# Kernel optimization log

Measured on AMD Instinct MI355X. Metric: run time of the kernel, lower is better.

The kernel has to match this reference:

```python
import jax, jax.numpy as jnp
from jax import lax
import numpy as np

# ---- static APPM geometry (MMAL-Net config: input 448, stride 32 -> 14x14 fm) ----
STRIDE = 32
FM = 14
RATIOS = [[4, 4], [3, 5], [5, 3],
          [6, 6], [5, 7], [7, 5],
          [8, 8], [6, 10], [10, 6], [7, 9], [9, 7], [7, 10], [10, 7]]
N_LIST = [3, 2, 1]          # proposals per ratio-group -> proposalN = 6
IOU_THRESHS = [0.25, 0.25, 0.25]
GROUP_RATIO_SPLITS = [3, 6, 13]  # ratios 0:3, 3:6, 6:13


def _window_num(r):
    return (FM - r[0] + 1) * (FM - r[1] + 1)


def _build_coords():
    # indices2coordinates: window (i,j) of ratio (rh,rw) -> pixel box, inclusive ends
    coords = []
    for rh, rw in RATIOS:
        rows, cols = FM - rh + 1, FM - rw + 1
        ii, jj = np.meshgrid(np.arange(rows), np.arange(cols), indexing='ij')
        x0 = ii.reshape(-1) * STRIDE
        y0 = jj.reshape(-1) * STRIDE
        x1 = x0 + rh * STRIDE - 1
        y1 = y0 + rw * STRIDE - 1
        coords.append(np.stack([x0, y0, x1, y1], 1))
    return np.concatenate(coords, 0).astype(np.float32)

COORDS = jnp.asarray(_build_coords())  # [917, 4]
WINDOW_NUMS = [_window_num(r) for r in RATIOS]
_g1 = sum(WINDOW_NUMS[:3]); _g2 = sum(WINDOW_NUMS[3:6]); _g3 = sum(WINDOW_NUMS[6:])
GROUPS = [(0, _g1), (_g1, _g1 + _g2), (_g1 + _g2, _g1 + _g2 + _g3)]  # (0,361),(361,602),(602,917)


def _argmax_mask(logits):
    # mask = 0.7 everywhere, 1.0 at per-row argmax
    B, C = logits.shape
    one_hot = jax.nn.one_hot(jnp.argmax(logits, axis=1), C, dtype=logits.dtype)
    return 0.7 + 0.3 * one_hot


def _nms_group(scores, coords, n_pick, thresh):
    # greedy descending-score NMS; scores [W], coords [W,4]
    x0, y0, x1, y1 = coords[:, 0], coords[:, 1], coords[:, 2], coords[:, 3]
    areas = (x1 - x0 + 1.0) * (y1 - y0 + 1.0)

    def step(carry, _):
        valid, last = carry
        masked = jnp.where(valid, scores, -jnp.inf)
        idx = jnp.argmax(masked).astype(jnp.int32)
        idx = jnp.where(valid.any(), idx, last)  # pad by repeating last pick
        ix0, iy0, ix1, iy1 = coords[idx]
        lx = jnp.minimum(x1, ix1) - jnp.maximum(x0, ix0) + 1.0
        ly = jnp.minimum(y1, iy1) - jnp.maximum(y0, iy0) + 1.0
        inter = jnp.where((lx < 0) | (ly < 0), 0.0, lx * ly)
        iou = inter / (areas + areas[idx] - inter)
        valid = valid & (iou <= thresh)  # also suppresses idx itself (iou == 1)
        return (valid, idx), idx

    init = (jnp.ones(scores.shape[0], dtype=bool), jnp.int32(0))
    (_, _), picks = lax.scan(step, init, None, length=n_pick)
    return picks  # [n_pick] int32


def _appm(local_fm):
    # avgpool over each ratio then sum over channels == channel-sum then 2D mean pool
    B = local_fm.shape[0]
    fm_sum = jnp.sum(local_fm, axis=1)  # [B,14,14]
    per_ratio = []
    for rh, rw in RATIOS:
        pooled = lax.reduce_window(fm_sum, jnp.float32(0.0), lax.add,
                                   (1, rh, rw), (1, 1, 1), 'VALID') / (rh * rw)
        per_ratio.append(pooled.reshape(B, -1))
    all_scores = jnp.concatenate(per_ratio, axis=1)  # [B, 917]

    picks = []
    for (s, e), n_pick, thr in zip(GROUPS, N_LIST, IOU_THRESHS):
        g = jax.vmap(lambda sc: _nms_group(sc, COORDS[s:e], n_pick, thr))(all_scores[:, s:e])
        picks.append(g + s)
    proposalN_indices = jnp.concatenate(picks, axis=1)  # [B, 6]
    proposalN_windows_scores = jnp.take_along_axis(all_scores, proposalN_indices, axis=1)
    return proposalN_indices, proposalN_windows_scores, all_scores


def setup_inputs() -> dict:
    key = jax.random.key(0)
    ks = jax.random.split(key, 6)
    B, C, NC, BIT = 256, 512, 200, 48
    return {
        'local_fm': jax.random.normal(ks[0], (B, C, 14, 14), jnp.float32),
        'local_embeddings': jax.random.normal(ks[1], (B, C), jnp.float32),
        'W_cls': jax.random.normal(ks[2], (NC, C), jnp.float32) * 0.02,
        'b_cls': jax.random.normal(ks[3], (NC,), jnp.float32) * 0.02,
        'W_hash': jax.random.normal(ks[4], (BIT, NC), jnp.float32) * 0.02,
        'b_hash': jax.random.normal(ks[5], (BIT,), jnp.float32) * 0.02,
    }


def reference(local_fm, local_embeddings, W_cls, b_cls, W_hash, b_hash):
    # classification head + per-row argmax masking + hash head (Tanh)
    local_logits = local_embeddings @ W_cls.T + b_cls          # [B, num_classes]
    masked = local_logits * _argmax_mask(local_logits)
    local_hash_code = jnp.tanh(masked @ W_hash.T + b_hash)     # [B, bit]
    # APPM region proposal on detached feature map
    proposalN_indices, proposalN_windows_scores, window_scores = _appm(
        lax.stop_gradient(local_fm))
    return (local_hash_code, local_logits, proposalN_indices,
            proposalN_windows_scores, window_scores)
```

## Files before the change

### kernel.cpp

```cpp
#include <hip/hip_runtime.h>
#include <math.h>

#define NW 917

__constant__ int c_off[13]  = {0,121,241,361,442,522,602,651,696,741,789,837,877};
__constant__ int c_rh[13]   = {4,3,5,6,5,7,8,6,10,7,9,7,10};
__constant__ int c_rw[13]   = {4,5,3,6,7,5,8,10,6,9,7,10,7};
__constant__ int c_cols[13] = {11,10,12,9,8,10,7,5,9,6,8,5,8};

__device__ inline void decode_w(int w, int& r, int& i, int& j){
    int rr = 0;
    #pragma unroll
    for (int k = 1; k < 13; ++k) if (w >= c_off[k]) rr = k;
    int loc = w - c_off[rr];
    int cols = c_cols[rr];
    r = rr; i = loc / cols; j = loc - i * cols;
}

__global__ __launch_bounds__(512) void chansum_kernel(const float* __restrict__ fm,
                                                      float* __restrict__ fmsum){
    int b = blockIdx.x;
    int t = threadIdx.x;
    int sub = t >> 6, lane = t & 63;
    __shared__ float4 red[8][49];
    const float4* base = (const float4*)(fm + (size_t)b * 512 * 196);
    if (lane < 49){
        float4 acc = {0.f,0.f,0.f,0.f};
        int c0 = sub * 64;
        #pragma unroll 8
        for (int c = 0; c < 64; ++c){
            float4 v = base[(size_t)(c0 + c) * 49 + lane];
            acc.x += v.x; acc.y += v.y; acc.z += v.z; acc.w += v.w;
        }
        red[sub][lane] = acc;
    }
    __syncthreads();
    if (t < 49){
        float4 s = red[0][t];
        #pragma unroll
        for (int k = 1; k < 8; ++k){
            float4 v = red[k][t];
            s.x += v.x; s.y += v.y; s.z += v.z; s.w += v.w;
        }
        ((float4*)fmsum)[b * 49 + t] = s;
    }
}

__global__ __launch_bounds__(256) void appm_kernel(const float* __restrict__ fmsum,
                                                   float* __restrict__ out_scores,
                                                   float* __restrict__ out_idx,
                                                   float* __restrict__ out_psc){
    int b = blockIdx.x, t = threadIdx.x;
    __shared__ float fm[196];
    __shared__ float R[14][15];
    __shared__ float I[15][15];
    __shared__ float s[NW];
    __shared__ float rv[256];
    __shared__ int   ri[256];

    if (t < 196) fm[t] = fmsum[b * 196 + t];
    __syncthreads();
    if (t < 14){
        float run = 0.f;
        R[t][0] = 0.f;
        for (int j = 0; j < 14; ++j){ run += fm[t * 14 + j]; R[t][j + 1] = run; }
    }
    __syncthreads();
    if (t < 15){
        float run = 0.f;
        I[0][t] = 0.f;
        for (int i = 0; i < 14; ++i){ run += R[i][t]; I[i + 1][t] = run; }
    }
    __syncthreads();
    for (int w = t; w < NW; w += 256){
        int r, i, j; decode_w(w, r, i, j);
        int rh = c_rh[r], rw = c_rw[r];
        float sum = I[i + rh][j + rw] - I[i][j + rw] - I[i + rh][j] + I[i][j];
        float sc = sum / (float)(rh * rw);
        s[w] = sc;
        out_scores[(size_t)b * NW + w] = sc;
    }
    __syncthreads();

    const int gs_[3] = {0, 361, 602};
    const int ge_[3] = {361, 602, NW};
    const int np_[3] = {3, 2, 1};
    int slot = 0;
    for (int g = 0; g < 3; ++g){
        int gs = gs_[g], ge = ge_[g];
        int w0 = gs + t, w1 = gs + t + 256;
        bool has0 = w0 < ge, has1 = w1 < ge;
        float x00=0,y00=0,x10=0,y10=0,a0=1.f;
        float x01=0,y01=0,x11=0,y11=0,a1=1.f;
        if (has0){
            int r,i,j; decode_w(w0,r,i,j);
            x00 = i*32.f; y00 = j*32.f;
            x10 = x00 + c_rh[r]*32.f - 1.f; y10 = y00 + c_rw[r]*32.f - 1.f;
            a0  = (float)(c_rh[r]*32 * c_rw[r]*32);
        }
        if (has1){
            int r,i,j; decode_w(w1,r,i,j);
            x01 = i*32.f; y01 = j*32.f;
            x11 = x01 + c_rh[r]*32.f - 1.f; y11 = y01 + c_rw[r]*32.f - 1.f;
            a1  = (float)(c_rh[r]*32 * c_rw[r]*32);
        }
        bool v0 = true, v1 = true;
        int last = 0;
        for (int p = 0; p < np_[g]; ++p){
            float bv = -INFINITY; int bi = 0x7fffffff;
            if (has0 && v0){ bv = s[w0]; bi = w0; }
            if (has1 && v1){ float sv = s[w1]; if (sv > bv){ bv = sv; bi = w1; } }
            rv[t] = bv; ri[t] = bi;
            __syncthreads();
            for (int st = 128; st > 0; st >>= 1){
                if (t < st){
                    float ov = rv[t + st]; int oi = ri[t + st];
                    if (ov > rv[t] || (ov == rv[t] && oi < ri[t])){ rv[t] = ov; ri[t] = oi; }
                }
                __syncthreads();
            }
            float mv = rv[0];
            int pick = (mv == -INFINITY) ? last : ri[0];
            __syncthreads();
            last = pick;
            int pr, pi, pj; decode_w(pick, pr, pi, pj);
            float px0 = pi*32.f, py0 = pj*32.f;
            float px1 = px0 + c_rh[pr]*32.f - 1.f, py1 = py0 + c_rw[pr]*32.f - 1.f;
            float pa  = (float)(c_rh[pr]*32 * c_rw[pr]*32);
            if (has0 && v0){
                float lx = fminf(x10,px1) - fmaxf(x00,px0) + 1.f;
                float ly = fminf(y10,py1) - fmaxf(y00,py0) + 1.f;
                float inter = (lx < 0.f || ly < 0.f) ? 0.f : lx * ly;
                float iou = inter / (a0 + pa - inter);
                v0 = (iou <= 0.25f);
            }
            if (has1 && v1){
                float lx = fminf(x11,px1) - fmaxf(x01,px0) + 1.f;
                float ly = fminf(y11,py1) - fmaxf(y01,py0) + 1.f;
                float inter = (lx < 0.f || ly < 0.f) ? 0.f : lx * ly;
                float iou = inter / (a1 + pa - inter);
                v1 = (iou <= 0.25f);
            }
            if (t == 0){
                out_idx[b * 6 + slot] = (float)pick;
                out_psc[b * 6 + slot] = s[pick];
            }
            slot++;
        }
    }
}

__global__ __launch_bounds__(256) void cls_kernel(const float* __restrict__ E,
                                                  const float* __restrict__ Wc,
                                                  const float* __restrict__ bc,
                                                  const float* __restrict__ Wh,
                                                  const float* __restrict__ bh,
                                                  float* __restrict__ out_hash,
                                                  float* __restrict__ out_logits){
    int b = blockIdx.x, t = threadIdx.x;
    __shared__ float emb[512];
    __shared__ float lg[200];
    __shared__ float mk[200];
    __shared__ float rv[256];
    __shared__ int   ri[256];
    emb[t]       = E[b * 512 + t];
    emb[t + 256] = E[b * 512 + 256 + t];
    __syncthreads();
    float lv = -INFINITY;
    if (t < 200){
        const float4* w4 = (const float4*)(Wc + (size_t)t * 512);
        float acc = bc[t];
        #pragma unroll 16
        for (int k = 0; k < 128; ++k){
            float4 w = w4[k];
            acc += emb[4*k]*w.x + emb[4*k+1]*w.y + emb[4*k+2]*w.z + emb[4*k+3]*w.w;
        }
        lg[t] = acc;
        out_logits[(size_t)b * 200 + t] = acc;
        lv = acc;
    }
    rv[t] = lv; ri[t] = t;
    __syncthreads();
    for (int st = 128; st > 0; st >>= 1){
        if (t < st){
            float ov = rv[t + st]; int oi = ri[t + st];
            if (ov > rv[t] || (ov == rv[t] && oi < ri[t])){ rv[t] = ov; ri[t] = oi; }
        }
        __syncthreads();
    }
    int amax = ri[0];
    if (t < 200) mk[t] = lg[t] * (t == amax ? 1.0f : 0.7f);
    __syncthreads();
    if (t < 48){
        const float4* w4 = (const float4*)(Wh + (size_t)t * 200);
        float acc = bh[t];
        #pragma unroll
        for (int k = 0; k < 50; ++k){
            float4 w = w4[k];
            acc += mk[4*k]*w.x + mk[4*k+1]*w.y + mk[4*k+2]*w.z + mk[4*k+3]*w.w;
        }
        out_hash[b * 48 + t] = tanhf(acc);
    }
}

extern "C" void kernel_launch(void* const* d_in, const int* in_sizes, int n_in,
                              void* d_out, int out_size, void* d_ws, size_t ws_size,
                              hipStream_t stream) {
    const float* fm = (const float*)d_in[0];
    const float* E  = (const float*)d_in[1];
    const float* Wc = (const float*)d_in[2];
    const float* bc = (const float*)d_in[3];
    const float* Wh = (const float*)d_in[4];
    const float* bh = (const float*)d_in[5];
    float* out        = (float*)d_out;
    float* out_hash   = out;
    float* out_logits = out + 12288;
    float* out_idx    = out + 63488;
    float* out_psc    = out + 65024;
    float* out_scores = out + 66560;
    float* fmsum = (float*)d_ws;

    hipLaunchKernelGGL(chansum_kernel, dim3(256), dim3(512), 0, stream, fm, fmsum);
    hipLaunchKernelGGL(appm_kernel,    dim3(256), dim3(256), 0, stream, fmsum,
                       out_scores, out_idx, out_psc);
    hipLaunchKernelGGL(cls_kernel,     dim3(256), dim3(256), 0, stream, E, Wc, bc, Wh, bh,
                       out_hash, out_logits);
}
```

Baseline: 198.8 us.

## Split channel sum across more blocks, fuse classifier head, use wave-shuffle argmax

```diff
diff --git a/kernel.cpp b/kernel.cpp
--- a/kernel.cpp
+++ b/kernel.cpp
@@ -17,48 +17,120 @@
     r = rr; i = loc / cols; j = loc - i * cols;
 }
 
-__global__ __launch_bounds__(512) void chansum_kernel(const float* __restrict__ fm,
-                                                      float* __restrict__ fmsum){
-    int b = blockIdx.x;
+__device__ inline unsigned long long nms_key(float v, int w){
+    unsigned u = __float_as_uint(v);
+    u = (u & 0x80000000u) ? ~u : (u | 0x80000000u);
+    return ((unsigned long long)u << 32) | (unsigned)(0xFFFFFFFFu - (unsigned)w);
+}
+
+__device__ inline unsigned long long shfl_xor_u64(unsigned long long x, int m){
+    unsigned lo = (unsigned)x, hi = (unsigned)(x >> 32);
+    lo = __shfl_xor(lo, m);
+    hi = __shfl_xor(hi, m);
+    return ((unsigned long long)hi << 32) | lo;
+}
+
+__global__ __launch_bounds__(256) void fused1_kernel(const float* __restrict__ fm,
+                                                     const float* __restrict__ E,
+                                                     const float* __restrict__ Wc,
+                                                     const float* __restrict__ bc,
+                                                     const float* __restrict__ Wh,
+                                                     const float* __restrict__ bh,
+                                                     float* __restrict__ partial,
+                                                     float* __restrict__ out_hash,
+                                                     float* __restrict__ out_logits){
     int t = threadIdx.x;
-    int sub = t >> 6, lane = t & 63;
-    __shared__ float4 red[8][49];
-    const float4* base = (const float4*)(fm + (size_t)b * 512 * 196);
-    if (lane < 49){
-        float4 acc = {0.f,0.f,0.f,0.f};
-        int c0 = sub * 64;
-        #pragma unroll 8
-        for (int c = 0; c < 64; ++c){
-            float4 v = base[(size_t)(c0 + c) * 49 + lane];
-            acc.x += v.x; acc.y += v.y; acc.z += v.z; acc.w += v.w;
-        }
-        red[sub][lane] = acc;
-    }
-    __syncthreads();
-    if (t < 49){
-        float4 s = red[0][t];
+    int lane = t & 63, wv = t >> 6;
+    if (blockIdx.x < 1024){
+        int b = blockIdx.x >> 2, part = blockIdx.x & 3;
+        __shared__ float4 red[4][49];
+        const float4* base = (const float4*)(fm + (size_t)b * 512 * 196)
+                             + (size_t)(part * 128) * 49;
+        if (lane < 49){
+            float4 acc = {0.f,0.f,0.f,0.f};
+            int c0 = wv * 32;
+            #pragma unroll 8
+            for (int k = 0; k < 32; ++k){
+                float4 v = base[(size_t)(c0 + k) * 49 + lane];
+                acc.x += v.x; acc.y += v.y; acc.z += v.z; acc.w += v.w;
+            }
+            red[wv][lane] = acc;
+        }
+        __syncthreads();
+        if (t < 49){
+            float4 s0 = red[0][t], s1 = red[1][t], s2 = red[2][t], s3 = red[3][t];
+            float4 s;
+            s.x = (s0.x + s1.x) + (s2.x + s3.x);
+            s.y = (s0.y + s1.y) + (s2.y + s3.y);
+            s.z = (s0.z + s1.z) + (s2.z + s3.z);
+            s.w = (s0.w + s1.w) + (s2.w + s3.w);
+            ((float4*)partial)[(blockIdx.x) * 49 + t] = s;
+        }
+    } else {
+        int b = blockIdx.x - 1024;
+        __shared__ float emb[512];
+        __shared__ float lg[200];
+        __shared__ float mk[200];
+        __shared__ unsigned long long wredc[4];
+        emb[t]       = E[b * 512 + t];
+        emb[t + 256] = E[b * 512 + 256 + t];
+        __syncthreads();
+        float lv = 0.f;
+        if (t < 200){
+            const float4* w4 = (const float4*)(Wc + (size_t)t * 512);
+            float acc = bc[t];
+            #pragma unroll 16
+            for (int k = 0; k < 128; ++k){
+                float4 w = w4[k];
+                acc += emb[4*k]*w.x + emb[4*k+1]*w.y + emb[4*k+2]*w.z + emb[4*k+3]*w.w;
+            }
+            lg[t] = acc;
+            out_logits[(size_t)b * 200 + t] = acc;
+            lv = acc;
+        }
+        unsigned long long key = (t < 200) ? nms_key(lv, t) : 0ULL;
         #pragma unroll
-        for (int k = 1; k < 8; ++k){
-            float4 v = red[k][t];
-            s.x += v.x; s.y += v.y; s.z += v.z; s.w += v.w;
-        }
-        ((float4*)fmsum)[b * 49 + t] = s;
-    }
-}
-
-__global__ __launch_bounds__(256) void appm_kernel(const float* __restrict__ fmsum,
+        for (int off = 32; off > 0; off >>= 1){
+            unsigned long long o = shfl_xor_u64(key, off);
+            if (o > key) key = o;
+        }
+        if (lane == 0) wredc[wv] = key;
+        __syncthreads();
+        unsigned long long ka = wredc[0] > wredc[1] ? wredc[0] : wredc[1];
+        unsigned long long kb = wredc[2] > wredc[3] ? wredc[2] : wredc[3];
+        if (kb > ka) ka = kb;
+        int amax = (int)(0xFFFFFFFFu - (unsigned)(ka & 0xFFFFFFFFu));
+        if (t < 200) mk[t] = lg[t] * (t == amax ? 1.0f : 0.7f);
+        __syncthreads();
+        if (t < 48){
+            const float4* w4 = (const float4*)(Wh + (size_t)t * 200);
+            float acc = bh[t];
+            #pragma unroll
+            for (int k = 0; k < 50; ++k){
+                float4 w = w4[k];
+                acc += mk[4*k]*w.x + mk[4*k+1]*w.y + mk[4*k+2]*w.z + mk[4*k+3]*w.w;
+            }
+            out_hash[b * 48 + t] = tanhf(acc);
+        }
+    }
+}
+
+__global__ __launch_bounds__(256) void appm_kernel(const float* __restrict__ partial,
                                                    float* __restrict__ out_scores,
                                                    float* __restrict__ out_idx,
                                                    float* __restrict__ out_psc){
     int b = blockIdx.x, t = threadIdx.x;
+    int lane = t & 63, wv = t >> 6;
     __shared__ float fm[196];
     __shared__ float R[14][15];
     __shared__ float I[15][15];
     __shared__ float s[NW];
-    __shared__ float rv[256];
-    __shared__ int   ri[256];
-
-    if (t < 196) fm[t] = fmsum[b * 196 + t];
+    __shared__ unsigned long long wred[4];
+
+    if (t < 196){
+        const float* p = partial + (size_t)b * 784 + t;
+        fm[t] = (p[0] + p[196]) + (p[392] + p[588]);
+    }
     __syncthreads();
     if (t < 14){
         float run = 0.f;
@@ -107,20 +179,24 @@
         bool v0 = true, v1 = true;
         int last = 0;
         for (int p = 0; p < np_[g]; ++p){
-            float bv = -INFINITY; int bi = 0x7fffffff;
-            if (has0 && v0){ bv = s[w0]; bi = w0; }
-            if (has1 && v1){ float sv = s[w1]; if (sv > bv){ bv = sv; bi = w1; } }
-            rv[t] = bv; ri[t] = bi;
+            unsigned long long key = 0ULL;
+            if (has0 && v0) key = nms_key(s[w0], w0);
+            if (has1 && v1){
+                unsigned long long k2 = nms_key(s[w1], w1);
+                if (k2 > key) key = k2;
+            }
+            #pragma unroll
+            for (int off = 32; off > 0; off >>= 1){
+                unsigned long long o = shfl_xor_u64(key, off);
+                if (o > key) key = o;
+            }
+            if (lane == 0) wred[wv] = key;
             __syncthreads();
-            for (int st = 128; st > 0; st >>= 1){
-                if (t < st){
-                    float ov = rv[t + st]; int oi = ri[t + st];
-                    if (ov > rv[t] || (ov == rv[t] && oi < ri[t])){ rv[t] = ov; ri[t] = oi; }
-                }
-                __syncthreads();
-            }
-            float mv = rv[0];
-            int pick = (mv == -INFINITY) ? last : ri[0];
+            unsigned long long ka = wred[0] > wred[1] ? wred[0] : wred[1];
+            unsigned long long kb = wred[2] > wred[3] ? wred[2] : wred[3];
+            if (kb > ka) ka = kb;
+            int pick = (ka == 0ULL) ? last
+                                    : (int)(0xFFFFFFFFu - (unsigned)(ka & 0xFFFFFFFFu));
             __syncthreads();
             last = pick;
             int pr, pi, pj; decode_w(pick, pr, pi, pj);
@@ -147,59 +223,6 @@
             }
             slot++;
         }
-    }
-}
-
-__global__ __launch_bounds__(256) void cls_kernel(const float* __restrict__ E,
-                                                  const float* __restrict__ Wc,
-                                                  const float* __restrict__ bc,
-                                                  const float* __restrict__ Wh,
-                                                  const float* __restrict__ bh,
-                                                  float* __restrict__ out_hash,
-                                                  float* __restrict__ out_logits){
-    int b = blockIdx.x, t = threadIdx.x;
-    __shared__ float emb[512];
-    __shared__ float lg[200];
-    __shared__ float mk[200];
-    __shared__ float rv[256];
-    __shared__ int   ri[256];
-    emb[t]       = E[b * 512 + t];
-    emb[t + 256] = E[b * 512 + 256 + t];
-    __syncthreads();
-    float lv = -INFINITY;
-    if (t < 200){
-        const float4* w4 = (const float4*)(Wc + (size_t)t * 512);
-        float acc = bc[t];
-        #pragma unroll 16
-        for (int k = 0; k < 128; ++k){
-            float4 w = w4[k];
-            acc += emb[4*k]*w.x + emb[4*k+1]*w.y + emb[4*k+2]*w.z + emb[4*k+3]*w.w;
-        }
-        lg[t] = acc;
-        out_logits[(size_t)b * 200 + t] = acc;
-        lv = acc;
-    }
-    rv[t] = lv; ri[t] = t;
-    __syncthreads();
-    for (int st = 128; st > 0; st >>= 1){
-        if (t < st){
-            float ov = rv[t + st]; int oi = ri[t + st];
-            if (ov > rv[t] || (ov == rv[t] && oi < ri[t])){ rv[t] = ov; ri[t] = oi; }
-        }
-        __syncthreads();
-    }
-    int amax = ri[0];
-    if (t < 200) mk[t] = lg[t] * (t == amax ? 1.0f : 0.7f);
-    __syncthreads();
-    if (t < 48){
-        const float4* w4 = (const float4*)(Wh + (size_t)t * 200);
-        float acc = bh[t];
-        #pragma unroll
-        for (int k = 0; k < 50; ++k){
-            float4 w = w4[k];
-            acc += mk[4*k]*w.x + mk[4*k+1]*w.y + mk[4*k+2]*w.z + mk[4*k+3]*w.w;
-        }
-        out_hash[b * 48 + t] = tanhf(acc);
     }
 }
 
@@ -218,11 +241,10 @@
     float* out_idx    = out + 63488;
     float* out_psc    = out + 65024;
     float* out_scores = out + 66560;
-    float* fmsum = (float*)d_ws;
-
-    hipLaunchKernelGGL(chansum_kernel, dim3(256), dim3(512), 0, stream, fm, fmsum);
-    hipLaunchKernelGGL(appm_kernel,    dim3(256), dim3(256), 0, stream, fmsum,
-                       out_scores, out_idx, out_psc);
-    hipLaunchKernelGGL(cls_kernel,     dim3(256), dim3(256), 0, stream, E, Wc, bc, Wh, bh,
-                       out_hash, out_logits);
-}
+    float* partial    = (float*)d_ws;
+
+    hipLaunchKernelGGL(fused1_kernel, dim3(1280), dim3(256), 0, stream,
+                       fm, E, Wc, bc, Wh, bh, partial, out_hash, out_logits);
+    hipLaunchKernelGGL(appm_kernel,   dim3(256),  dim3(256), 0, stream,
+                       partial, out_scores, out_idx, out_psc);
+}
```

Result: faster. 187.3 us (-5.8%).
